# Kernel optimization log

Hardware: AMD Instinct MI355X
Metric: run time of the kernel (lower is better)

Reference implementation:

```python
import jax, jax.numpy as jnp
import numpy as np

B, C = 8192, 4096

def setup_inputs() -> dict:
    key = jax.random.key(0)
    k0, k1, k2, k3 = jax.random.split(key, 4)
    x = jax.random.normal(k0, (B, C), dtype=jnp.float32)
    target = jax.random.randint(k1, (B,), 0, C, dtype=jnp.int32)
    # distance_rank[t] is the list of class indices ranked by wordnet distance
    # from class t; emulate with a random permutation per row.
    scores = jax.random.uniform(k2, (C, C))
    distance_rank = jnp.argsort(scores, axis=1).astype(jnp.int32)
    # k = randint(class_index + 1, class_num - 1) inclusive, per (batch, class_index)
    c = jnp.arange(2, C - 1)  # class_index values, [C-3]
    span = (C - 1) - (c + 1) + 1  # number of valid k values per class_index
    u = jax.random.uniform(k3, (B, C - 3))
    k_idx = (c + 1 + jnp.floor(u * span)).astype(jnp.int32)
    k_idx = jnp.minimum(k_idx, C - 1)
    return {"x": x, "target": target, "distance_rank": distance_rank, "k_idx": k_idx}


def reference(x, target, distance_rank, k_idx):
    Bn, Cn = x.shape
    alpha = jnp.float32(Cn - 1)  # len(input[0]) - 1
    ranks = distance_rank[target]  # [B, C] class ids ranked by distance from target
    yi = jnp.take_along_axis(x, ranks[:, 1:2], axis=1)        # [B, 1]
    yj = jnp.take_along_axis(x, ranks[:, 2:Cn - 1], axis=1)   # [B, C-3]
    yk_cls = jnp.take_along_axis(ranks, k_idx, axis=1)        # [B, C-3]
    yk = jnp.take_along_axis(x, yk_cls, axis=1)               # [B, C-3]
    # mid = (1 + (yi - y)^2/alpha)^(-(alpha+1)/2); computed in log space for
    # stability (exponent is -(C)/2, direct pow underflows)
    e = -(alpha + 1.0) / 2.0
    la = e * jnp.log1p((yi - yj) ** 2 / alpha)
    lb = e * jnp.log1p((yi - yk) ** 2 / alpha)
    # log2(pijk) = (log midij - log(midij + midik)) / ln 2
    log2_pijk = (la - jnp.logaddexp(la, lb)) / jnp.log(jnp.float32(2.0))
    ctste = jnp.sum(log2_pijk)
    sc = -ctste / Bn / (Cn - 1)
    # F.cross_entropy(input, target), mean reduction
    logp = jax.nn.log_softmax(x, axis=1)
    ce = -jnp.mean(jnp.take_along_axis(logp, target[:, None], axis=1))
    theta = jnp.float32(0.6)
    return theta * ce + (1.0 - theta) * sc
```

## Files before the change

### kernel.cpp

```cpp
#include <hip/hip_runtime.h>
#include <math.h>

constexpr int BN = 8192;
constexpr int CN = 4096;
constexpr int NT = 256;
constexpr int NW = NT / 64;
constexpr int V4 = CN / (NT * 4);

__device__ __forceinline__ unsigned bf16_rne(float f) {
    const unsigned u = __float_as_uint(f);
    return (u + 0x7FFFu + ((u >> 16) & 1u)) >> 16;
}

__global__ __launch_bounds__(NT, 8) void sc_row_kernel(
    const float* __restrict__ x,
    const int*   __restrict__ target,
    const int*   __restrict__ distance_rank,
    const int*   __restrict__ k_idx,
    float*       __restrict__ ws)
{
    __shared__ unsigned short xsb[CN];
    __shared__ unsigned short qlp[CN];
    __shared__ float red_s[NW];

    const int b    = blockIdx.x;
    const int tid  = threadIdx.x;
    const int lane = tid & 63;
    const int wave = tid >> 6;

    const int t = target[b];
    const float* __restrict__ xrow = x + (size_t)b * CN;
    const int*   __restrict__ drow = distance_rank + (size_t)t * CN;
    const int*   __restrict__ krow = k_idx + (size_t)b * (CN - 3);

    float sl = 0.f;
    #pragma unroll
    for (int i = 0; i < V4; ++i) {
        const float4 v = reinterpret_cast<const float4*>(xrow)[tid + i * NT];
        sl += __expf(v.x) + __expf(v.y) + __expf(v.z) + __expf(v.w);
        uint2 st;
        st.x = bf16_rne(v.x) | (bf16_rne(v.y) << 16);
        st.y = bf16_rne(v.z) | (bf16_rne(v.w) << 16);
        reinterpret_cast<uint2*>(xsb)[tid + i * NT] = st;
    }
    const float xt  = xrow[t];
    const int   rk1 = drow[1];
    const float yi  = xrow[rk1];

    #pragma unroll
    for (int off = 32; off; off >>= 1) sl += __shfl_down(sl, off, 64);
    if (lane == 0) red_s[wave] = sl;

    __syncthreads();

    if (tid == 0) {
        float sg = red_s[0];
        #pragma unroll
        for (int w = 1; w < NW; ++w) sg += red_s[w];
        ws[4 * BN + b] = __logf(sg) - xt;
    }

    const float alpha = (float)(CN - 1);
    const float QS = 1048576.0f;
    const float C0 = 0.5f - 11.9996480f * QS;
    int qv[V4][4];
    #pragma unroll
    for (int i = 0; i < V4; ++i) {
        const int4 rv = reinterpret_cast<const int4*>(drow)[tid + i * NT];
        const float d0 = yi - __uint_as_float((unsigned)xsb[rv.x] << 16);
        const float d1 = yi - __uint_as_float((unsigned)xsb[rv.y] << 16);
        const float d2 = yi - __uint_as_float((unsigned)xsb[rv.z] << 16);
        const float d3 = yi - __uint_as_float((unsigned)xsb[rv.w] << 16);
        const float L0 = __log2f(fmaf(d0, d0, alpha));
        const float L1 = __log2f(fmaf(d1, d1, alpha));
        const float L2 = __log2f(fmaf(d2, d2, alpha));
        const float L3 = __log2f(fmaf(d3, d3, alpha));
        qv[i][0] = min(max((int)fmaf(L0, QS, C0), 0), 65535);
        qv[i][1] = min(max((int)fmaf(L1, QS, C0), 0), 65535);
        qv[i][2] = min(max((int)fmaf(L2, QS, C0), 0), 65535);
        qv[i][3] = min(max((int)fmaf(L3, QS, C0), 0), 65535);
        uint2 st;
        st.x = (unsigned)qv[i][0] | ((unsigned)qv[i][1] << 16);
        st.y = (unsigned)qv[i][2] | ((unsigned)qv[i][3] << 16);
        reinterpret_cast<uint2*>(qlp)[tid + i * NT] = st;
    }
    __syncthreads();

    const float DS = 0.001953125f;
    float acc = 0.f;
    #pragma unroll
    for (int i = 0; i < V4; ++i) {
        #pragma unroll
        for (int q = 0; q < 4; ++q) {
            const int  c    = 4 * tid + 1024 * i + q;
            const bool vjok = (c >= 2) && (c <= CN - 2);
            const int  jj   = vjok ? (c - 2) : 0;
            const int  kk   = krow[jj];
            const int  qk   = (int)qlp[kk];
            const float D   = (float)(qv[i][q] - qk) * DS;
            const float term = __log2f(1.0f + __builtin_amdgcn_exp2f(D));
            acc -= vjok ? term : 0.f;
        }
    }
    #pragma unroll
    for (int off = 32; off; off >>= 1) acc += __shfl_down(acc, off, 64);
    if (lane == 0) ws[4 * b + wave] = acc;
}

__global__ __launch_bounds__(1024) void sc_finalize(
    const float* __restrict__ ws, float* __restrict__ out)
{
    __shared__ double dred[32];
    const int tid  = threadIdx.x;
    const int lane = tid & 63;
    const int wave = tid >> 6;

    double sc = 0.0, ce = 0.0;
    for (int i = tid; i < 4 * BN; i += 1024) sc += (double)ws[i];
    for (int i = tid; i < BN; i += 1024)     ce += (double)ws[4 * BN + i];
    for (int off = 32; off; off >>= 1) {
        sc += __shfl_down(sc, off, 64);
        ce += __shfl_down(ce, off, 64);
    }
    if (lane == 0) { dred[wave] = sc; dred[16 + wave] = ce; }
    __syncthreads();
    if (tid == 0) {
        double scs = 0.0, ces = 0.0;
        #pragma unroll
        for (int w = 0; w < 16; ++w) { scs += dred[w]; ces += dred[16 + w]; }
        double ce_mean = ces / (double)BN;
        double sc_val  = -scs / (double)BN / (double)(CN - 1);
        out[0] = (float)(0.6 * ce_mean + 0.4 * sc_val);
    }
}

extern "C" void kernel_launch(void* const* d_in, const int* in_sizes, int n_in,
                              void* d_out, int out_size, void* d_ws, size_t ws_size,
                              hipStream_t stream) {
    const float* x             = (const float*)d_in[0];
    const int*   target        = (const int*)d_in[1];
    const int*   distance_rank = (const int*)d_in[2];
    const int*   k_idx         = (const int*)d_in[3];
    float*       ws            = (float*)d_ws;

    sc_row_kernel<<<BN, NT, 0, stream>>>(x, target, distance_rank, k_idx, ws);
    sc_finalize<<<1, 1024, 0, stream>>>(ws, (float*)d_out);
}
```

Measured before the change: 76.74 us.

## Process each row with a single wavefront, dropping block-level barriers

Each row is now handled by one 64-lane wavefront instead of a 256-thread block. That removes the __syncthreads calls and the shared-memory reduction, relying on s_waitcnt plus a sched_barrier to order LDS accesses within the wave. The third phase now reads its j-side values from LDS (qlp[j+2]) instead of keeping them in registers, and walks k_idx with a lane-strided, coalesced pattern. The workspace layout shrinks to one partial sum per row. The trade-off is more serial work per wave and the same 16KB of LDS per one-wave block, which may limit how many waves each CU can hold and hide latency.

```diff
diff --git a/kernel.cpp b/kernel.cpp
--- a/kernel.cpp
+++ b/kernel.cpp
@@ -3,16 +3,14 @@
 
 constexpr int BN = 8192;
 constexpr int CN = 4096;
-constexpr int NT = 256;
-constexpr int NW = NT / 64;
-constexpr int V4 = CN / (NT * 4);
+constexpr int NT = 64;
 
 __device__ __forceinline__ unsigned bf16_rne(float f) {
     const unsigned u = __float_as_uint(f);
     return (u + 0x7FFFu + ((u >> 16) & 1u)) >> 16;
 }
 
-__global__ __launch_bounds__(NT, 8) void sc_row_kernel(
+__global__ __launch_bounds__(NT) void sc_row_kernel(
     const float* __restrict__ x,
     const int*   __restrict__ target,
     const int*   __restrict__ distance_rank,
@@ -21,12 +19,9 @@
 {
     __shared__ unsigned short xsb[CN];
     __shared__ unsigned short qlp[CN];
-    __shared__ float red_s[NW];
 
     const int b    = blockIdx.x;
-    const int tid  = threadIdx.x;
-    const int lane = tid & 63;
-    const int wave = tid >> 6;
+    const int lane = threadIdx.x;
 
     const int t = target[b];
     const float* __restrict__ xrow = x + (size_t)b * CN;
@@ -35,13 +30,13 @@
 
     float sl = 0.f;
     #pragma unroll
-    for (int i = 0; i < V4; ++i) {
-        const float4 v = reinterpret_cast<const float4*>(xrow)[tid + i * NT];
+    for (int i = 0; i < 16; ++i) {
+        const float4 v = reinterpret_cast<const float4*>(xrow)[lane + i * 64];
         sl += __expf(v.x) + __expf(v.y) + __expf(v.z) + __expf(v.w);
         uint2 st;
         st.x = bf16_rne(v.x) | (bf16_rne(v.y) << 16);
         st.y = bf16_rne(v.z) | (bf16_rne(v.w) << 16);
-        reinterpret_cast<uint2*>(xsb)[tid + i * NT] = st;
+        reinterpret_cast<uint2*>(xsb)[lane + i * 64] = st;
     }
     const float xt  = xrow[t];
     const int   rk1 = drow[1];
@@ -49,24 +44,18 @@
 
     #pragma unroll
     for (int off = 32; off; off >>= 1) sl += __shfl_down(sl, off, 64);
-    if (lane == 0) red_s[wave] = sl;
+    if (lane == 0) ws[BN + b] = __logf(sl) - xt;
 
-    __syncthreads();
-
-    if (tid == 0) {
-        float sg = red_s[0];
-        #pragma unroll
-        for (int w = 1; w < NW; ++w) sg += red_s[w];
-        ws[4 * BN + b] = __logf(sg) - xt;
-    }
+    asm volatile("s_waitcnt lgkmcnt(0)" ::: "memory");
+    __builtin_amdgcn_sched_barrier(0);
 
     const float alpha = (float)(CN - 1);
     const float QS = 1048576.0f;
     const float C0 = 0.5f - 11.9996480f * QS;
-    int qv[V4][4];
-    #pragma unroll
-    for (int i = 0; i < V4; ++i) {
-        const int4 rv = reinterpret_cast<const int4*>(drow)[tid + i * NT];
+    #pragma unroll 4
+    for (int i = 0; i < 16; ++i) {
+        const int p = lane + i * 64;
+        const int4 rv = reinterpret_cast<const int4*>(drow)[p];
         const float d0 = yi - __uint_as_float((unsigned)xsb[rv.x] << 16);
         const float d1 = yi - __uint_as_float((unsigned)xsb[rv.y] << 16);
         const float d2 = yi - __uint_as_float((unsigned)xsb[rv.z] << 16);
@@ -75,36 +64,35 @@
         const float L1 = __log2f(fmaf(d1, d1, alpha));
         const float L2 = __log2f(fmaf(d2, d2, alpha));
         const float L3 = __log2f(fmaf(d3, d3, alpha));
-        qv[i][0] = min(max((int)fmaf(L0, QS, C0), 0), 65535);
-        qv[i][1] = min(max((int)fmaf(L1, QS, C0), 0), 65535);
-        qv[i][2] = min(max((int)fmaf(L2, QS, C0), 0), 65535);
-        qv[i][3] = min(max((int)fmaf(L3, QS, C0), 0), 65535);
+        const int q0 = min(max((int)fmaf(L0, QS, C0), 0), 65535);
+        const int q1 = min(max((int)fmaf(L1, QS, C0), 0), 65535);
+        const int q2 = min(max((int)fmaf(L2, QS, C0), 0), 65535);
+        const int q3 = min(max((int)fmaf(L3, QS, C0), 0), 65535);
         uint2 st;
-        st.x = (unsigned)qv[i][0] | ((unsigned)qv[i][1] << 16);
-        st.y = (unsigned)qv[i][2] | ((unsigned)qv[i][3] << 16);
-        reinterpret_cast<uint2*>(qlp)[tid + i * NT] = st;
+        st.x = (unsigned)q0 | ((unsigned)q1 << 16);
+        st.y = (unsigned)q2 | ((unsigned)q3 << 16);
+        reinterpret_cast<uint2*>(qlp)[p] = st;
     }
-    __syncthreads();
+    asm volatile("s_waitcnt lgkmcnt(0)" ::: "memory");
+    __builtin_amdgcn_sched_barrier(0);
 
     const float DS = 0.001953125f;
     float acc = 0.f;
-    #pragma unroll
-    for (int i = 0; i < V4; ++i) {
-        #pragma unroll
-        for (int q = 0; q < 4; ++q) {
-            const int  c    = 4 * tid + 1024 * i + q;
-            const bool vjok = (c >= 2) && (c <= CN - 2);
-            const int  jj   = vjok ? (c - 2) : 0;
-            const int  kk   = krow[jj];
-            const int  qk   = (int)qlp[kk];
-            const float D   = (float)(qv[i][q] - qk) * DS;
-            const float term = __log2f(1.0f + __builtin_amdgcn_exp2f(D));
-            acc -= vjok ? term : 0.f;
-        }
+    #pragma unroll 4
+    for (int m = 0; m < 64; ++m) {
+        const int  j  = lane + m * 64;
+        const bool ok = (j <= CN - 4);
+        const int  jj = ok ? j : (CN - 4);
+        const int  kk = krow[jj];
+        const int  qj = (int)qlp[jj + 2];
+        const int  qk = (int)qlp[kk];
+        const float D = (float)(qj - qk) * DS;
+        const float term = __log2f(1.0f + __builtin_amdgcn_exp2f(D));
+        acc -= ok ? term : 0.f;
     }
     #pragma unroll
     for (int off = 32; off; off >>= 1) acc += __shfl_down(acc, off, 64);
-    if (lane == 0) ws[4 * b + wave] = acc;
+    if (lane == 0) ws[b] = acc;
 }
 
 __global__ __launch_bounds__(1024) void sc_finalize(
@@ -116,8 +104,10 @@
     const int wave = tid >> 6;
 
     double sc = 0.0, ce = 0.0;
-    for (int i = tid; i < 4 * BN; i += 1024) sc += (double)ws[i];
-    for (int i = tid; i < BN; i += 1024)     ce += (double)ws[4 * BN + i];
+    for (int i = tid; i < BN; i += 1024) {
+        sc += (double)ws[i];
+        ce += (double)ws[BN + i];
+    }
     for (int off = 32; off; off >>= 1) {
         sc += __shfl_down(sc, off, 64);
         ce += __shfl_down(ce, off, 64);
```

Result: slower. 91.81 us (+19.6%).
